# Optimization experiments

Hardware: AMD Instinct MI355X
Metric: run time of the kernel (lower is better)

Reference implementation:

```python
import jax, jax.numpy as jnp
import numpy as np

IMG = 256
CUT_RATE = 0.1
CUT_LEN = int(IMG * CUT_RATE)      # 25
REMAIN = (IMG - CUT_LEN) // 2      # 115
CROP = 2 * REMAIN                  # 230  (crop window is always CROP x CROP)


def _cut_start(index):
    # vectorized cut_location(); window length is always CROP, return left edge a
    xy = IMG - index
    return jnp.where(index <= REMAIN, 0,
           jnp.where(xy <= REMAIN, IMG - CROP, index - REMAIN)).astype(jnp.int32)


def _bilinear_crop(img, x0, y0):
    # img: [C, IMG, IMG]; crop CROP x CROP window at (x0, y0) and resize to
    # IMG x IMG with bilinear, align_corners=True (matches F.interpolate).
    scale = (CROP - 1) / (IMG - 1)
    src = jnp.arange(IMG, dtype=img.dtype) * scale        # [IMG] source coords in crop
    i0 = jnp.floor(src).astype(jnp.int32)
    i1 = jnp.minimum(i0 + 1, CROP - 1)
    w = src - i0.astype(img.dtype)                        # [IMG] frac weights
    r0, r1 = x0 + i0, x0 + i1                             # absolute row indices
    c0, c1 = y0 + i0, y0 + i1                             # absolute col indices
    top = img[:, r0, :]                                   # [C, IMG, IMG]
    bot = img[:, r1, :]
    rows = top * (1.0 - w)[None, :, None] + bot * w[None, :, None]
    left = rows[:, :, c0]
    right = rows[:, :, c1]
    return left * (1.0 - w)[None, None, :] + right * w[None, None, :]


def setup_inputs() -> dict:
    key = jax.random.key(0)
    k1, k2 = jax.random.split(key)
    x = jax.random.normal(k1, (128, 3, 256, 256), dtype=jnp.float32)
    feature_map = jax.random.normal(k2, (128, 512, 16, 16), dtype=jnp.float32)
    return {"x": x, "feature_map": feature_map}


def reference(x, feature_map):
    B, C, H, W = feature_map.shape
    # SE-style weighting: global avg pool per channel, relu(weight * fm)
    fw = feature_map.mean(axis=(2, 3), keepdims=True)     # [B,C,1,1]
    se = jax.nn.relu(fw * feature_map)                    # [B,C,H,W]
    cam = se.mean(axis=1)                                 # [B,H,W] channel-mean CAM
    idx = jnp.argmax(cam.reshape(B, -1), axis=1)          # flat argmax per sample
    fx = idx // H                                         # torch uses feature_size[0]
    fy = idx % W
    ix = (IMG * fx) // H                                  # map to image coords
    iy = (IMG * fy) // W
    x_left = _cut_start(ix)
    y_top = _cut_start(iy)
    out = jax.vmap(_bilinear_crop)(x, x_left, y_top)      # [B,3,256,256]
    # torch clones+detaches the crop; output carries no gradient
    return jax.lax.stop_gradient(out)
```

## Files before the change

### kernel.cpp

```cpp
#include <hip/hip_runtime.h>

#define IMG 256
#define CROPW 230
#define REMAIN 115
#define NGROUP 16
#define GCH    32
#define TILE_I 16
#define MAXROWS 16
#define NTILE  16

__device__ __forceinline__ int cut_start(int v) {
    int xy = IMG - v;
    return (v <= REMAIN) ? 0 : ((xy <= REMAIN) ? (IMG - CROPW) : (v - REMAIN));
}

__global__ __launch_bounds__(256) void cam_partial_kernel(
    const float* __restrict__ fm, float* __restrict__ cam_part)
{
    const int blk = blockIdx.x;
    const int b = blk >> 4;
    const int g = blk & (NGROUP - 1);
    const int tid = threadIdx.x;
    const int lane = tid & 63;
    const int wave = tid >> 6;

    __shared__ float tile[GCH * 256];
    __shared__ float fw[GCH];

    const float* src = fm + ((size_t)b * 512 + (size_t)g * GCH) * 256;

    const float4* src4 = (const float4*)src;
    float4* tile4 = (float4*)tile;
    #pragma unroll
    for (int k = 0; k < 8; ++k)
        tile4[tid + k * 256] = src4[tid + k * 256];
    __syncthreads();

    for (int c = wave * 8; c < wave * 8 + 8; ++c) {
        const float* row = tile + c * 256;
        float s = row[lane] + row[lane + 64] + row[lane + 128] + row[lane + 192];
        #pragma unroll
        for (int off = 32; off >= 1; off >>= 1)
            s += __shfl_xor(s, off, 64);
        if (lane == 0) fw[c] = s * (1.0f / 256.0f);
    }
    __syncthreads();

    float acc = 0.0f;
    #pragma unroll
    for (int c = 0; c < GCH; ++c) {
        float v = fw[c] * tile[c * 256 + tid];
        acc += (v > 0.0f) ? v : 0.0f;
    }
    cam_part[(size_t)blk * 256 + tid] = acc;
}

__global__ __launch_bounds__(256) void argmax_kernel(
    const float* __restrict__ cam_part, int* __restrict__ se_out)
{
    const int b = blockIdx.x;
    const int tid = threadIdx.x;

    __shared__ float s_val[256];
    __shared__ int   s_idx[256];

    float acc = 0.0f;
    #pragma unroll
    for (int g = 0; g < NGROUP; ++g)
        acc += cam_part[((size_t)b * NGROUP + g) * 256 + tid];

    s_val[tid] = acc;
    s_idx[tid] = tid;
    __syncthreads();

    for (int stride = 128; stride >= 1; stride >>= 1) {
        if (tid < stride) {
            float v2 = s_val[tid + stride]; int i2 = s_idx[tid + stride];
            float v1 = s_val[tid];          int i1 = s_idx[tid];
            if (v2 > v1 || (v2 == v1 && i2 < i1)) { s_val[tid] = v2; s_idx[tid] = i2; }
        }
        __syncthreads();
    }

    if (tid == 0) {
        int idx = s_idx[0];
        int fx = idx >> 4, fy = idx & 15;
        int ix = 16 * fx,  iy = 16 * fy;
        se_out[2 * b]     = cut_start(ix);
        se_out[2 * b + 1] = cut_start(iy);
    }
}

__global__ __launch_bounds__(256) void bilinear_tiled_kernel(
    const float* __restrict__ x, const int* __restrict__ se, float* __restrict__ out)
{
    __shared__ float rows[MAXROWS * 256];

    const int bx = blockIdx.x;
    const int bc = bx >> 4;
    const int ib = (bx & 15) * TILE_I;
    const int b  = bc / 3;
    const int tid = threadIdx.x;

    const int x0 = se[2 * b];
    const int y0 = se[2 * b + 1];

    const float scale = (float)(229.0 / 255.0);

    const int i0_first = (int)floorf((float)ib * scale);
    const int r_first  = x0 + i0_first;

    {
        const float4* src4 = (const float4*)(x + (size_t)bc * (IMG * IMG));
        float4* rows4 = (float4*)rows;
        const int wave = tid >> 6;
        const int lane = tid & 63;
        #pragma unroll
        for (int k = 0; k < 4; ++k) {
            const int row  = 4 * k + wave;
            const int srow = min(r_first + row, IMG - 1);
            rows4[tid + k * 256] = src4[srow * 64 + lane];
        }
    }
    __syncthreads();

    const int jp  = tid & 127;
    const int ilh = tid >> 7;

    const int   ja  = 2 * jp;
    const float sja = (float)ja * scale;
    const int   j0a = (int)floorf(sja);
    const float wja = sja - (float)j0a;
    const int   c0a = y0 + j0a;

    const int   jb  = ja + 1;
    const float sjb = (float)jb * scale;
    const int   j0b = (int)floorf(sjb);
    const float wjb = sjb - (float)j0b;
    const int   c1b = y0 + min(j0b + 1, CROPW - 1);
    const bool  bstep = (j0b != j0a);

    float2* outp2 = (float2*)(out + (size_t)bc * (IMG * IMG) + (size_t)ib * IMG) + jp;

    #pragma unroll
    for (int iter = 0; iter < TILE_I / 2; ++iter) {
        const int   il = 2 * iter + ilh;
        const int   i  = ib + il;
        const float si = (float)i * scale;
        const int   i0 = (int)floorf(si);
        const float wi = si - (float)i0;
        const int   i1 = min(i0 + 1, CROPW - 1);
        const int   row0 = (x0 + i0 - r_first) << 8;
        const int   row1 = (x0 + i1 - r_first) << 8;
        const float owi = 1.0f - wi;

        const float t0 = rows[row0 + c0a];
        const float t1 = rows[row0 + c0a + 1];
        const float tx = rows[row0 + c1b];
        const float u0 = rows[row1 + c0a];
        const float u1 = rows[row1 + c0a + 1];
        const float ux = rows[row1 + c1b];

        const float la = t0 * owi + u0 * wi;
        const float ra = t1 * owi + u1 * wi;
        const float oa = la * (1.0f - wja) + ra * wja;

        const float tb = bstep ? t1 : t0;
        const float ub = bstep ? u1 : u0;
        const float lb = tb * owi + ub * wi;
        const float rb = tx * owi + ux * wi;
        const float ob = lb * (1.0f - wjb) + rb * wjb;

        outp2[il * 128] = make_float2(oa, ob);
    }
}

extern "C" void kernel_launch(void* const* d_in, const int* in_sizes, int n_in,
                              void* d_out, int out_size, void* d_ws, size_t ws_size,
                              hipStream_t stream) {
    const float* x  = (const float*)d_in[0];
    const float* fm = (const float*)d_in[1];
    float* out = (float*)d_out;

    int*   se       = (int*)d_ws;
    float* cam_part = (float*)((char*)d_ws + 1024);

    cam_partial_kernel<<<128 * NGROUP, 256, 0, stream>>>(fm, cam_part);
    argmax_kernel<<<128, 256, 0, stream>>>(cam_part, se);

    bilinear_tiled_kernel<<<384 * NTILE, 256, 0, stream>>>(x, se, out);
}
```

Measured before the change: 53.46 us.

## Double-buffer bilinear tiles with direct global-to-LDS loads across three tiles per block

The bilinear kernel now handles three tiles per block. It prefetches the next tile's source rows into a second LDS buffer using global_load_lds DMA while the current tile is being interpolated. The goal is to hide global load latency and avoid routing loads through registers. In exchange, LDS use doubles, the grid has fewer blocks, and the loop waits on vmcnt(0), which also covers outstanding stores, so prefetch overlap may be limited.

```diff
diff --git a/kernel.cpp b/kernel.cpp
--- a/kernel.cpp
+++ b/kernel.cpp
@@ -8,10 +8,18 @@
 #define TILE_I 16
 #define MAXROWS 16
 #define NTILE  16
+#define TPB    3
 
 __device__ __forceinline__ int cut_start(int v) {
     int xy = IMG - v;
     return (v <= REMAIN) ? 0 : ((xy <= REMAIN) ? (IMG - CROPW) : (v - REMAIN));
+}
+
+__device__ __forceinline__ void load_row16(const float* g, float* l) {
+    __builtin_amdgcn_global_load_lds(
+        (const __attribute__((address_space(1))) void*)g,
+        (__attribute__((address_space(3))) void*)l,
+        16, 0, 0);
 }
 
 __global__ __launch_bounds__(256) void cam_partial_kernel(
@@ -91,87 +99,114 @@
     }
 }
 
-__global__ __launch_bounds__(256) void bilinear_tiled_kernel(
+__global__ __launch_bounds__(256) void bilinear_dma_kernel(
     const float* __restrict__ x, const int* __restrict__ se, float* __restrict__ out)
 {
-    __shared__ float rows[MAXROWS * 256];
-
-    const int bx = blockIdx.x;
-    const int bc = bx >> 4;
-    const int ib = (bx & 15) * TILE_I;
-    const int b  = bc / 3;
-    const int tid = threadIdx.x;
-
-    const int x0 = se[2 * b];
-    const int y0 = se[2 * b + 1];
-
+    __shared__ float buf[2][MAXROWS * 256];
+
+    const int tid  = threadIdx.x;
+    const int wave = tid >> 6;
+    const int lane = tid & 63;
     const float scale = (float)(229.0 / 255.0);
 
-    const int i0_first = (int)floorf((float)ib * scale);
-    const int r_first  = x0 + i0_first;
+    const int t0 = blockIdx.x * TPB;
+    const int jp  = tid & 127;
+    const int ilh = tid >> 7;
 
     {
-        const float4* src4 = (const float4*)(x + (size_t)bc * (IMG * IMG));
-        float4* rows4 = (float4*)rows;
-        const int wave = tid >> 6;
-        const int lane = tid & 63;
+        const int bc = t0 >> 4;
+        const int ib = (t0 & (NTILE - 1)) * TILE_I;
+        const int b  = bc / 3;
+        const int x0 = se[2 * b];
+        const int r_first = x0 + (int)floorf((float)ib * scale);
+        const float* img = x + (size_t)bc * (IMG * IMG);
         #pragma unroll
         for (int k = 0; k < 4; ++k) {
-            const int row  = 4 * k + wave;
-            const int srow = min(r_first + row, IMG - 1);
-            rows4[tid + k * 256] = src4[srow * 64 + lane];
-        }
-    }
-    __syncthreads();
-
-    const int jp  = tid & 127;
-    const int ilh = tid >> 7;
-
-    const int   ja  = 2 * jp;
-    const float sja = (float)ja * scale;
-    const int   j0a = (int)floorf(sja);
-    const float wja = sja - (float)j0a;
-    const int   c0a = y0 + j0a;
-
-    const int   jb  = ja + 1;
-    const float sjb = (float)jb * scale;
-    const int   j0b = (int)floorf(sjb);
-    const float wjb = sjb - (float)j0b;
-    const int   c1b = y0 + min(j0b + 1, CROPW - 1);
-    const bool  bstep = (j0b != j0a);
-
-    float2* outp2 = (float2*)(out + (size_t)bc * (IMG * IMG) + (size_t)ib * IMG) + jp;
-
-    #pragma unroll
-    for (int iter = 0; iter < TILE_I / 2; ++iter) {
-        const int   il = 2 * iter + ilh;
-        const int   i  = ib + il;
-        const float si = (float)i * scale;
-        const int   i0 = (int)floorf(si);
-        const float wi = si - (float)i0;
-        const int   i1 = min(i0 + 1, CROPW - 1);
-        const int   row0 = (x0 + i0 - r_first) << 8;
-        const int   row1 = (x0 + i1 - r_first) << 8;
-        const float owi = 1.0f - wi;
-
-        const float t0 = rows[row0 + c0a];
-        const float t1 = rows[row0 + c0a + 1];
-        const float tx = rows[row0 + c1b];
-        const float u0 = rows[row1 + c0a];
-        const float u1 = rows[row1 + c0a + 1];
-        const float ux = rows[row1 + c1b];
-
-        const float la = t0 * owi + u0 * wi;
-        const float ra = t1 * owi + u1 * wi;
-        const float oa = la * (1.0f - wja) + ra * wja;
-
-        const float tb = bstep ? t1 : t0;
-        const float ub = bstep ? u1 : u0;
-        const float lb = tb * owi + ub * wi;
-        const float rb = tx * owi + ux * wi;
-        const float ob = lb * (1.0f - wjb) + rb * wjb;
-
-        outp2[il * 128] = make_float2(oa, ob);
+            const int r = wave * 4 + k;
+            const int srow = min(r_first + r, IMG - 1);
+            load_row16(img + srow * IMG + lane * 4, &buf[0][r * 256]);
+        }
+    }
+    asm volatile("s_waitcnt vmcnt(0)" ::: "memory");
+    __syncthreads();
+
+    for (int it = 0; it < TPB; ++it) {
+        const int t   = t0 + it;
+        const int cur = it & 1;
+        const int bc  = t >> 4;
+        const int ib  = (t & (NTILE - 1)) * TILE_I;
+        const int b   = bc / 3;
+        const int x0  = se[2 * b];
+        const int y0  = se[2 * b + 1];
+        const int r_first = x0 + (int)floorf((float)ib * scale);
+
+        if (it + 1 < TPB) {
+            const int tn  = t + 1;
+            const int bcn = tn >> 4;
+            const int ibn = (tn & (NTILE - 1)) * TILE_I;
+            const int bn  = bcn / 3;
+            const int x0n = se[2 * bn];
+            const int rfn = x0n + (int)floorf((float)ibn * scale);
+            const float* imgn = x + (size_t)bcn * (IMG * IMG);
+            #pragma unroll
+            for (int k = 0; k < 4; ++k) {
+                const int r = wave * 4 + k;
+                const int srow = min(rfn + r, IMG - 1);
+                load_row16(imgn + srow * IMG + lane * 4, &buf[cur ^ 1][r * 256]);
+            }
+        }
+
+        const float* rows = buf[cur];
+
+        const int   ja  = 2 * jp;
+        const float sja = (float)ja * scale;
+        const int   j0a = (int)floorf(sja);
+        const float wja = sja - (float)j0a;
+        const int   c0a = y0 + j0a;
+
+        const int   jb  = ja + 1;
+        const float sjb = (float)jb * scale;
+        const int   j0b = (int)floorf(sjb);
+        const float wjb = sjb - (float)j0b;
+        const int   c1b = y0 + min(j0b + 1, CROPW - 1);
+        const bool  bstep = (j0b != j0a);
+
+        float2* outp2 = (float2*)(out + (size_t)bc * (IMG * IMG) + (size_t)ib * IMG) + jp;
+
+        #pragma unroll
+        for (int iter = 0; iter < TILE_I / 2; ++iter) {
+            const int   il = 2 * iter + ilh;
+            const int   i  = ib + il;
+            const float si = (float)i * scale;
+            const int   i0 = (int)floorf(si);
+            const float wi = si - (float)i0;
+            const int   i1 = min(i0 + 1, CROPW - 1);
+            const int   row0 = (x0 + i0 - r_first) << 8;
+            const int   row1 = (x0 + i1 - r_first) << 8;
+            const float owi = 1.0f - wi;
+
+            const float t0v = rows[row0 + c0a];
+            const float t1v = rows[row0 + c0a + 1];
+            const float txv = rows[row0 + c1b];
+            const float u0v = rows[row1 + c0a];
+            const float u1v = rows[row1 + c0a + 1];
+            const float uxv = rows[row1 + c1b];
+
+            const float la = t0v * owi + u0v * wi;
+            const float ra = t1v * owi + u1v * wi;
+            const float oa = la * (1.0f - wja) + ra * wja;
+
+            const float tb = bstep ? t1v : t0v;
+            const float ub = bstep ? u1v : u0v;
+            const float lb = tb * owi + ub * wi;
+            const float rb = txv * owi + uxv * wi;
+            const float ob = lb * (1.0f - wjb) + rb * wjb;
+
+            outp2[il * 128] = make_float2(oa, ob);
+        }
+
+        asm volatile("s_waitcnt vmcnt(0)" ::: "memory");
+        __syncthreads();
     }
 }
 
@@ -188,5 +223,5 @@
     cam_partial_kernel<<<128 * NGROUP, 256, 0, stream>>>(fm, cam_part);
     argmax_kernel<<<128, 256, 0, stream>>>(cam_part, se);
 
-    bilinear_tiled_kernel<<<384 * NTILE, 256, 0, stream>>>(x, se, out);
-}
+    bilinear_dma_kernel<<<2048, 256, 0, stream>>>(x, se, out);
+}
```

Result: no change. 53.52 us (+0.1%).
